# Kernel tuning notes

Measured on AMD Instinct MI355X. Metric: run time of the kernel, lower is better.

Reference implementation:

```python
import jax, jax.numpy as jnp
import numpy as np

BATCH = 64
FEAT = 2048          # backbone.out_features (ResNet-50)
C = 112              # bottleneck_dim = number of concepts
E = 512              # concept_emb_dim
NUM_CLASSES = 345


def setup_inputs() -> dict:
    key = jax.random.key(0)
    ks = jax.random.split(key, 7)
    s_emb = 1.0 / np.sqrt(FEAT)
    s_p = 1.0 / np.sqrt(2 * E)
    s_h = 1.0 / np.sqrt(C * E)
    return {
        "x": jax.random.normal(ks[0], (BATCH, FEAT), jnp.float32),
        "W_emb": jax.random.normal(ks[1], (C, FEAT, 2 * E), jnp.float32) * s_emb,
        "b_emb": jax.random.normal(ks[2], (C, 2 * E), jnp.float32) * s_emb,
        "W_pint": jax.random.normal(ks[3], (C, 2 * E), jnp.float32) * s_p,
        "b_pint": jax.random.normal(ks[4], (C,), jnp.float32) * s_p,
        "W_head": jax.random.normal(ks[5], (C * E, NUM_CLASSES), jnp.float32) * s_h,
        "b_head": jax.random.normal(ks[6], (NUM_CLASSES,), jnp.float32) * s_h,
    }


def reference(x, W_emb, b_emb, W_pint, b_pint, W_head, b_head):
    # Batched version of the per-concept Linear loop: [B,C,2E]
    embeddings = jnp.einsum("bf,cfe->bce", x, W_emb) + b_emb
    positive_embs = embeddings[..., :E]   # [B,C,E]
    negative_embs = embeddings[..., E:]   # [B,C,E]
    # Per-concept Linear(2E, 1) -> [B,C]
    p_int_logits = jnp.einsum("bce,ce->bc", embeddings, W_pint) + b_pint
    p_int_pos = jax.nn.sigmoid(p_int_logits)              # [B,C]
    p = p_int_pos[..., None]
    mixed_embs = p * positive_embs + (1.0 - p) * negative_embs  # [B,C,E]
    flattened = mixed_embs.reshape(mixed_embs.shape[0], -1)     # [B, C*E]
    final_preds = flattened @ W_head + b_head                   # [B, num_classes]
    return (final_preds, flattened, p_int_pos)
```

## Files before the change

### kernel.cpp

```cpp
#include <hip/hip_runtime.h>

typedef __attribute__((ext_vector_type(4))) float  f4;
typedef __attribute__((ext_vector_type(8))) short  bf16x8;
typedef __attribute__((ext_vector_type(4))) float  f32x4;
typedef __attribute__((ext_vector_type(4))) unsigned short us4;
typedef __attribute__((ext_vector_type(2))) unsigned int u32x2;

#define BATCH 64
#define FEAT 2048
#define NC_C 112
#define TE 1024
#define EE 512
#define NCLS 345
#define NCLSP 352
#define KHEAD 57344

__device__ __forceinline__ unsigned short f2bf(float f) {
    unsigned u = __float_as_uint(f);
    unsigned r = (u + 0x7FFFu + ((u >> 16) & 1u)) >> 16;
    return (unsigned short)r;
}
__device__ __forceinline__ float bf2f(unsigned short h) {
    return __uint_as_float(((unsigned)h) << 16);
}
__device__ __forceinline__ unsigned cvtpk(float a, float b) {
    unsigned r;
    asm("v_cvt_pk_bf16_f32 %0, %1, %2" : "=v"(r) : "v"(a), "v"(b));
    return r;
}

__global__ __launch_bounds__(256) void k_emb(
    const float* __restrict__ x, const float* __restrict__ W_emb,
    const float* __restrict__ b_emb, unsigned short* __restrict__ emb_bf)
{
    __shared__ __align__(16) unsigned short Alds[64 * 40];
    __shared__ __align__(16) unsigned short Blds[128 * 40];

    const int tid = threadIdx.x;
    const int c  = blockIdx.x >> 3;
    const int n0 = (blockIdx.x & 7) * 128;
    const float* __restrict__ Wc = W_emb + (size_t)c * (FEAT * TE);

    const int w = tid >> 6, l = tid & 63;
    const int mbase = (w & 1) * 32, nbase = (w >> 1) * 64;

    const int a_row = tid >> 3;
    const int a_k4  = (tid & 7) * 4;
    const int b_kp  = tid >> 4;
    const int b_n4  = (tid & 15) * 4;

    const float* __restrict__ axp = x + (size_t)a_row * FEAT + a_k4;
    const float* __restrict__ bpp = Wc + (size_t)(2 * b_kp) * TE + n0 + b_n4;

    unsigned short* __restrict__ aw0 = &Alds[a_row * 40 + a_k4];
    unsigned short* __restrict__ aw1 = &Alds[(a_row + 32) * 40 + a_k4];
    const int koct = b_kp >> 2, klo = (2 * b_kp) & 7;

    auto ke_load = [&](f4& A0, f4& A1, f4& B0, f4& B1, f4& B2, f4& B3, int kstep) {
        const float* ax_ = axp + kstep * 32;
        A0 = *(const f4*)ax_;
        A1 = *(const f4*)(ax_ + 32 * FEAT);
        const float* bp_ = bpp + (size_t)kstep * 32 * TE;
        B0 = *(const f4*)bp_;         B1 = *(const f4*)(bp_ + TE);
        B2 = *(const f4*)(bp_ + 64);  B3 = *(const f4*)(bp_ + TE + 64);
    };
    auto ke_write = [&](const f4& A0, const f4& A1, const f4& B0, const f4& B1,
                        const f4& B2, const f4& B3) {
        u32x2 v0, v1;
        v0[0] = cvtpk(A0[0], A0[1]); v0[1] = cvtpk(A0[2], A0[3]);
        v1[0] = cvtpk(A1[0], A1[1]); v1[1] = cvtpk(A1[2], A1[3]);
        *(u32x2*)aw0 = v0;
        *(u32x2*)aw1 = v1;
#pragma unroll
        for (int i = 0; i < 4; ++i) {
            int n = b_n4 + i;
            *(unsigned*)&Blds[n * 40 + (((koct ^ ((n >> 2) & 3)) << 3) | klo)] =
                cvtpk(B0[i], B1[i]);
            n += 64;
            *(unsigned*)&Blds[n * 40 + (((koct ^ ((n >> 2) & 3)) << 3) | klo)] =
                cvtpk(B2[i], B3[i]);
        }
    };

    f32x4 acc[2][4];
#pragma unroll
    for (int i = 0; i < 2; ++i)
#pragma unroll
        for (int j = 0; j < 4; ++j) acc[i][j] = (f32x4){0.f, 0.f, 0.f, 0.f};

    auto ke_mfma = [&]() {
        bf16x8 af[2], bfr[4];
#pragma unroll
        for (int si = 0; si < 2; ++si)
            af[si] = *(const bf16x8*)&Alds[(mbase + si * 16 + (l & 15)) * 40 + (l >> 4) * 8];
#pragma unroll
        for (int nf = 0; nf < 4; ++nf) {
            int n = nbase + nf * 16 + (l & 15);
            bfr[nf] = *(const bf16x8*)&Blds[n * 40 + (((l >> 4) ^ ((n >> 2) & 3)) << 3)];
        }
#pragma unroll
        for (int si = 0; si < 2; ++si)
#pragma unroll
            for (int nf = 0; nf < 4; ++nf)
                acc[si][nf] = __builtin_amdgcn_mfma_f32_16x16x32_bf16(
                    af[si], bfr[nf], acc[si][nf], 0, 0, 0);
    };

    f4 aA0, aA1, bA0, bA1, bA2, bA3;
    f4 aB0, aB1, bB0, bB1, bB2, bB3;
    ke_load(aA0, aA1, bA0, bA1, bA2, bA3, 0);
    ke_load(aB0, aB1, bB0, bB1, bB2, bB3, 1);

    for (int s = 0; s < 64; s += 2) {
        __syncthreads();
        ke_write(aA0, aA1, bA0, bA1, bA2, bA3);
        __syncthreads();
        if (s < 62) ke_load(aA0, aA1, bA0, bA1, bA2, bA3, s + 2);
        ke_mfma();

        __syncthreads();
        ke_write(aB0, aB1, bB0, bB1, bB2, bB3);
        __syncthreads();
        if (s < 61) ke_load(aB0, aB1, bB0, bB1, bB2, bB3, s + 3);
        ke_mfma();
    }

#pragma unroll
    for (int si = 0; si < 2; ++si)
#pragma unroll
        for (int nf = 0; nf < 4; ++nf) {
            const int nl = nbase + nf * 16 + (l & 15);
            const int ng = n0 + nl;
            const float bias = b_emb[c * TE + ng];
#pragma unroll
            for (int r = 0; r < 4; ++r) {
                const int bb = mbase + si * 16 + (l >> 4) * 4 + r;
                const float v = acc[si][nf][r] + bias;
                emb_bf[((size_t)bb * NC_C + c) * TE + ng] = f2bf(v);
            }
        }
}

__global__ __launch_bounds__(256) void k_mix(
    const unsigned short* __restrict__ emb_bf, const float* __restrict__ W_pint,
    const float* __restrict__ b_pint, float* __restrict__ flat_out,
    float* __restrict__ p_out)
{
    const int tid = threadIdx.x;
    const int l = tid & 63, w = tid >> 6;
    const int pidx = blockIdx.x * 4 + w;
    const int b = pidx / NC_C, c = pidx - b * NC_C;

    const unsigned short* __restrict__ row = emb_bf + ((size_t)b * NC_C + c) * TE;
    const float* __restrict__ wp = W_pint + c * TE;

    float vals[16];
    float dot = 0.f;
#pragma unroll
    for (int i = 0; i < 4; ++i) {
        const int e = 4 * l + 256 * i;
        us4 u = *(const us4*)&row[e];
        f4  wv = *(const f4*)&wp[e];
#pragma unroll
        for (int j = 0; j < 4; ++j) {
            float f = bf2f(u[j]);
            vals[i * 4 + j] = f;
            dot += f * wv[j];
        }
    }
#pragma unroll
    for (int m = 32; m >= 1; m >>= 1) dot += __shfl_xor(dot, m);
    const float logit = dot + b_pint[c];
    const float p = 1.f / (1.f + __expf(-logit));
    if (l == 0) p_out[b * NC_C + c] = p;

    float* __restrict__ fo = flat_out + (size_t)b * KHEAD + c * EE;
#pragma unroll
    for (int i = 0; i < 2; ++i) {
        const int e = 4 * l + 256 * i;
        f4 m;
#pragma unroll
        for (int j = 0; j < 4; ++j)
            m[j] = p * vals[i * 4 + j] + (1.f - p) * vals[(i + 2) * 4 + j];
        *(f4*)&fo[e] = m;
    }
}

__global__ __launch_bounds__(256) void k_head(
    const float* __restrict__ flat, const float* __restrict__ W_head,
    float* __restrict__ pbuf, int nsteps)
{
    __shared__ __align__(16) unsigned short Blds[NCLSP * 40];

    const int tid = threadIdx.x;
    const int w = tid >> 6, l = tid & 63;
    const int k0 = blockIdx.x * (nsteps * 32);

    f32x4 acc[22];
#pragma unroll
    for (int i = 0; i < 22; ++i) acc[i] = (f32x4){0.f, 0.f, 0.f, 0.f};

    for (int s = 0; s < nsteps; ++s) {
        const int kb = k0 + s * 32;
        __syncthreads();
        for (int idx = tid; idx < 32 * NCLSP; idx += 256) {
            const int k = idx / NCLSP;
            const int n = idx - k * NCLSP;
            const float v = (n < NCLS) ? W_head[(size_t)(kb + k) * NCLS + n] : 0.f;
            Blds[n * 40 + ((((k >> 3) ^ ((n >> 2) & 3)) << 3) | (k & 7))] = f2bf(v);
        }
        __syncthreads();

        const float* __restrict__ ap =
            flat + (size_t)(w * 16 + (l & 15)) * KHEAD + kb + (l >> 4) * 8;
        f4 af0 = *(const f4*)ap;
        f4 af1 = *(const f4*)(ap + 4);
        bf16x8 a;
        unsigned p0 = cvtpk(af0[0], af0[1]), p1 = cvtpk(af0[2], af0[3]);
        unsigned p2 = cvtpk(af1[0], af1[1]), p3 = cvtpk(af1[2], af1[3]);
        a[0] = (short)(p0 & 0xFFFF); a[1] = (short)(p0 >> 16);
        a[2] = (short)(p1 & 0xFFFF); a[3] = (short)(p1 >> 16);
        a[4] = (short)(p2 & 0xFFFF); a[5] = (short)(p2 >> 16);
        a[6] = (short)(p3 & 0xFFFF); a[7] = (short)(p3 >> 16);

#pragma unroll
        for (int nf = 0; nf < 22; ++nf) {
            const int n = nf * 16 + (l & 15);
            bf16x8 bfr = *(const bf16x8*)&Blds[n * 40 + (((l >> 4) ^ ((n >> 2) & 3)) << 3)];
            acc[nf] = __builtin_amdgcn_mfma_f32_16x16x32_bf16(a, bfr, acc[nf], 0, 0, 0);
        }
    }

    float* __restrict__ pb = pbuf + (size_t)blockIdx.x * (64 * NCLSP);
#pragma unroll
    for (int nf = 0; nf < 22; ++nf) {
        const int n = nf * 16 + (l & 15);
#pragma unroll
        for (int r = 0; r < 4; ++r) {
            const int row = w * 16 + (l >> 4) * 4 + r;
            pb[row * NCLSP + n] = acc[nf][r];
        }
    }
}

__global__ __launch_bounds__(256) void k_reduce(
    const float* __restrict__ pbuf, const float* __restrict__ b_head,
    float* __restrict__ final_out, int nb)
{
    const int i = blockIdx.x * 256 + threadIdx.x;
    if (i >= BATCH * NCLS) return;
    const int m = i / NCLS, n = i - m * NCLS;
    float s = b_head[n];
    for (int p = 0; p < nb; ++p)
        s += pbuf[((size_t)p * 64 + m) * NCLSP + n];
    final_out[i] = s;
}

extern "C" void kernel_launch(void* const* d_in, const int* in_sizes, int n_in,
                              void* d_out, int out_size, void* d_ws, size_t ws_size,
                              hipStream_t stream) {
    const float* x      = (const float*)d_in[0];
    const float* W_emb  = (const float*)d_in[1];
    const float* b_emb  = (const float*)d_in[2];
    const float* W_pint = (const float*)d_in[3];
    const float* b_pint = (const float*)d_in[4];
    const float* W_head = (const float*)d_in[5];
    const float* b_head = (const float*)d_in[6];

    float* out       = (float*)d_out;
    float* final_out = out;
    float* flat      = out + BATCH * NCLS;
    float* p_out     = out + BATCH * NCLS + BATCH * KHEAD;

    unsigned short* emb_bf = (unsigned short*)d_ws;
    float* pbuf = (float*)d_ws;

    int NB, nsteps;
    const size_t need224 = (size_t)224 * 64 * NCLSP * sizeof(float);
    if (ws_size >= need224) { NB = 224; nsteps = 8; }
    else                    { NB = 128; nsteps = 14; }

    k_emb<<<NC_C * 8, 256, 0, stream>>>(x, W_emb, b_emb, emb_bf);
    k_mix<<<(BATCH * NC_C) / 4, 256, 0, stream>>>(emb_bf, W_pint, b_pint, flat, p_out);
    k_head<<<NB, 256, 0, stream>>>(flat, W_head, pbuf, nsteps);
    k_reduce<<<(BATCH * NCLS + 255) / 256, 256, 0, stream>>>(pbuf, b_head, final_out, NB);
}
```

Baseline: 432.5 us.

## Pre-cast x to bf16 and stream W_emb directly into MFMA registers without LDS

Adds a small kernel that converts x to bf16 once, then rewrites the embedding GEMM so each wave loads its MFMA operand fragments straight from global memory into registers. LDS staging and all __syncthreads in the main loop go away, and a register double-buffered prefetch replaces them. The goal is to remove barrier and LDS round-trip overhead in this W_emb-bandwidth-bound kernel. The cost is scalar strided 4-byte loads of W_emb (eight rows per lane), which may coalesce worse than the earlier vectorized f4 loads, plus one extra kernel launch.

```diff
diff --git a/kernel.cpp b/kernel.cpp
--- a/kernel.cpp
+++ b/kernel.cpp
@@ -4,7 +4,7 @@
 typedef __attribute__((ext_vector_type(8))) short  bf16x8;
 typedef __attribute__((ext_vector_type(4))) float  f32x4;
 typedef __attribute__((ext_vector_type(4))) unsigned short us4;
-typedef __attribute__((ext_vector_type(2))) unsigned int u32x2;
+typedef __attribute__((ext_vector_type(4))) unsigned int u32x4;
 
 #define BATCH 64
 #define FEAT 2048
@@ -29,113 +29,102 @@
     return r;
 }
 
+__global__ __launch_bounds__(256) void k_xcast(
+    const float* __restrict__ x, unsigned short* __restrict__ xb)
+{
+    const int i = blockIdx.x * 256 + threadIdx.x;
+    const f4 v0 = *(const f4*)&x[i * 8];
+    const f4 v1 = *(const f4*)&x[i * 8 + 4];
+    u32x4 o;
+    o[0] = cvtpk(v0[0], v0[1]);
+    o[1] = cvtpk(v0[2], v0[3]);
+    o[2] = cvtpk(v1[0], v1[1]);
+    o[3] = cvtpk(v1[2], v1[3]);
+    *(u32x4*)&xb[i * 8] = o;
+}
+
 __global__ __launch_bounds__(256) void k_emb(
-    const float* __restrict__ x, const float* __restrict__ W_emb,
+    const unsigned short* __restrict__ xb, const float* __restrict__ W_emb,
     const float* __restrict__ b_emb, unsigned short* __restrict__ emb_bf)
 {
-    __shared__ __align__(16) unsigned short Alds[64 * 40];
-    __shared__ __align__(16) unsigned short Blds[128 * 40];
-
     const int tid = threadIdx.x;
     const int c  = blockIdx.x >> 3;
     const int n0 = (blockIdx.x & 7) * 128;
     const float* __restrict__ Wc = W_emb + (size_t)c * (FEAT * TE);
 
     const int w = tid >> 6, l = tid & 63;
-    const int mbase = (w & 1) * 32, nbase = (w >> 1) * 64;
-
-    const int a_row = tid >> 3;
-    const int a_k4  = (tid & 7) * 4;
-    const int b_kp  = tid >> 4;
-    const int b_n4  = (tid & 15) * 4;
-
-    const float* __restrict__ axp = x + (size_t)a_row * FEAT + a_k4;
-    const float* __restrict__ bpp = Wc + (size_t)(2 * b_kp) * TE + n0 + b_n4;
-
-    unsigned short* __restrict__ aw0 = &Alds[a_row * 40 + a_k4];
-    unsigned short* __restrict__ aw1 = &Alds[(a_row + 32) * 40 + a_k4];
-    const int koct = b_kp >> 2, klo = (2 * b_kp) & 7;
-
-    auto ke_load = [&](f4& A0, f4& A1, f4& B0, f4& B1, f4& B2, f4& B3, int kstep) {
-        const float* ax_ = axp + kstep * 32;
-        A0 = *(const f4*)ax_;
-        A1 = *(const f4*)(ax_ + 32 * FEAT);
-        const float* bp_ = bpp + (size_t)kstep * 32 * TE;
-        B0 = *(const f4*)bp_;         B1 = *(const f4*)(bp_ + TE);
-        B2 = *(const f4*)(bp_ + 64);  B3 = *(const f4*)(bp_ + TE + 64);
+    const int lm = l & 15, kg = l >> 4;
+    const int colbase = n0 + w * 32 + lm;
+
+    const float* __restrict__ bp = Wc + (size_t)(kg * 8) * TE + colbase;
+    const unsigned short* __restrict__ ap = xb + (size_t)lm * FEAT + kg * 8;
+
+    f32x4 acc[4][2];
+#pragma unroll
+    for (int mf = 0; mf < 4; ++mf)
+#pragma unroll
+        for (int nf = 0; nf < 2; ++nf) acc[mf][nf] = (f32x4){0.f, 0.f, 0.f, 0.f};
+
+    auto loadB = [&](float* B, int s) {
+        const float* p = bp + (size_t)s * 32 * TE;
+#pragma unroll
+        for (int nf = 0; nf < 2; ++nf)
+#pragma unroll
+            for (int r = 0; r < 8; ++r)
+                B[nf * 8 + r] = p[(size_t)r * TE + nf * 16];
     };
-    auto ke_write = [&](const f4& A0, const f4& A1, const f4& B0, const f4& B1,
-                        const f4& B2, const f4& B3) {
-        u32x2 v0, v1;
-        v0[0] = cvtpk(A0[0], A0[1]); v0[1] = cvtpk(A0[2], A0[3]);
-        v1[0] = cvtpk(A1[0], A1[1]); v1[1] = cvtpk(A1[2], A1[3]);
-        *(u32x2*)aw0 = v0;
-        *(u32x2*)aw1 = v1;
-#pragma unroll
-        for (int i = 0; i < 4; ++i) {
-            int n = b_n4 + i;
-            *(unsigned*)&Blds[n * 40 + (((koct ^ ((n >> 2) & 3)) << 3) | klo)] =
-                cvtpk(B0[i], B1[i]);
-            n += 64;
-            *(unsigned*)&Blds[n * 40 + (((koct ^ ((n >> 2) & 3)) << 3) | klo)] =
-                cvtpk(B2[i], B3[i]);
-        }
+    auto loadA = [&](bf16x8* A, int s) {
+        const unsigned short* p = ap + s * 32;
+#pragma unroll
+        for (int mf = 0; mf < 4; ++mf)
+            A[mf] = *(const bf16x8*)(p + mf * 16 * FEAT);
     };
-
-    f32x4 acc[2][4];
-#pragma unroll
-    for (int i = 0; i < 2; ++i)
-#pragma unroll
-        for (int j = 0; j < 4; ++j) acc[i][j] = (f32x4){0.f, 0.f, 0.f, 0.f};
-
-    auto ke_mfma = [&]() {
-        bf16x8 af[2], bfr[4];
-#pragma unroll
-        for (int si = 0; si < 2; ++si)
-            af[si] = *(const bf16x8*)&Alds[(mbase + si * 16 + (l & 15)) * 40 + (l >> 4) * 8];
-#pragma unroll
-        for (int nf = 0; nf < 4; ++nf) {
-            int n = nbase + nf * 16 + (l & 15);
-            bfr[nf] = *(const bf16x8*)&Blds[n * 40 + (((l >> 4) ^ ((n >> 2) & 3)) << 3)];
-        }
-#pragma unroll
-        for (int si = 0; si < 2; ++si)
-#pragma unroll
-            for (int nf = 0; nf < 4; ++nf)
-                acc[si][nf] = __builtin_amdgcn_mfma_f32_16x16x32_bf16(
-                    af[si], bfr[nf], acc[si][nf], 0, 0, 0);
+    auto compute = [&](const float* B, const bf16x8* A) {
+        bf16x8 bfr[2];
+#pragma unroll
+        for (int nf = 0; nf < 2; ++nf) {
+            u32x4 q;
+            q[0] = cvtpk(B[nf * 8 + 0], B[nf * 8 + 1]);
+            q[1] = cvtpk(B[nf * 8 + 2], B[nf * 8 + 3]);
+            q[2] = cvtpk(B[nf * 8 + 4], B[nf * 8 + 5]);
+            q[3] = cvtpk(B[nf * 8 + 6], B[nf * 8 + 7]);
+            bfr[nf] = __builtin_bit_cast(bf16x8, q);
+        }
+#pragma unroll
+        for (int mf = 0; mf < 4; ++mf)
+#pragma unroll
+            for (int nf = 0; nf < 2; ++nf)
+                acc[mf][nf] = __builtin_amdgcn_mfma_f32_16x16x32_bf16(
+                    A[mf], bfr[nf], acc[mf][nf], 0, 0, 0);
     };
 
-    f4 aA0, aA1, bA0, bA1, bA2, bA3;
-    f4 aB0, aB1, bB0, bB1, bB2, bB3;
-    ke_load(aA0, aA1, bA0, bA1, bA2, bA3, 0);
-    ke_load(aB0, aB1, bB0, bB1, bB2, bB3, 1);
-
+    float   Bc[16], Bn[16];
+    bf16x8  Ac[4],  An[4];
+    loadB(Bc, 0);
+    loadA(Ac, 0);
+
+#pragma unroll 1
     for (int s = 0; s < 64; s += 2) {
-        __syncthreads();
-        ke_write(aA0, aA1, bA0, bA1, bA2, bA3);
-        __syncthreads();
-        if (s < 62) ke_load(aA0, aA1, bA0, bA1, bA2, bA3, s + 2);
-        ke_mfma();
-
-        __syncthreads();
-        ke_write(aB0, aB1, bB0, bB1, bB2, bB3);
-        __syncthreads();
-        if (s < 61) ke_load(aB0, aB1, bB0, bB1, bB2, bB3, s + 3);
-        ke_mfma();
-    }
-
-#pragma unroll
-    for (int si = 0; si < 2; ++si)
-#pragma unroll
-        for (int nf = 0; nf < 4; ++nf) {
-            const int nl = nbase + nf * 16 + (l & 15);
-            const int ng = n0 + nl;
+        loadB(Bn, s + 1);
+        loadA(An, s + 1);
+        compute(Bc, Ac);
+        if (s + 2 < 64) {
+            loadB(Bc, s + 2);
+            loadA(Ac, s + 2);
+        }
+        compute(Bn, An);
+    }
+
+#pragma unroll
+    for (int mf = 0; mf < 4; ++mf)
+#pragma unroll
+        for (int nf = 0; nf < 2; ++nf) {
+            const int ng = n0 + w * 32 + nf * 16 + lm;
             const float bias = b_emb[c * TE + ng];
 #pragma unroll
             for (int r = 0; r < 4; ++r) {
-                const int bb = mbase + si * 16 + (l >> 4) * 4 + r;
-                const float v = acc[si][nf][r] + bias;
+                const int bb = mf * 16 + kg * 4 + r;
+                const float v = acc[mf][nf][r] + bias;
                 emb_bf[((size_t)bb * NC_C + c) * TE + ng] = f2bf(v);
             }
         }
@@ -215,13 +204,10 @@
             flat + (size_t)(w * 16 + (l & 15)) * KHEAD + kb + (l >> 4) * 8;
         f4 af0 = *(const f4*)ap;
         f4 af1 = *(const f4*)(ap + 4);
-        bf16x8 a;
-        unsigned p0 = cvtpk(af0[0], af0[1]), p1 = cvtpk(af0[2], af0[3]);
-        unsigned p2 = cvtpk(af1[0], af1[1]), p3 = cvtpk(af1[2], af1[3]);
-        a[0] = (short)(p0 & 0xFFFF); a[1] = (short)(p0 >> 16);
-        a[2] = (short)(p1 & 0xFFFF); a[3] = (short)(p1 >> 16);
-        a[4] = (short)(p2 & 0xFFFF); a[5] = (short)(p2 >> 16);
-        a[6] = (short)(p3 & 0xFFFF); a[7] = (short)(p3 >> 16);
+        u32x4 pq;
+        pq[0] = cvtpk(af0[0], af0[1]); pq[1] = cvtpk(af0[2], af0[3]);
+        pq[2] = cvtpk(af1[0], af1[1]); pq[3] = cvtpk(af1[2], af1[3]);
+        bf16x8 a = __builtin_bit_cast(bf16x8, pq);
 
 #pragma unroll
         for (int nf = 0; nf < 22; ++nf) {
@@ -274,13 +260,15 @@
 
     unsigned short* emb_bf = (unsigned short*)d_ws;
     float* pbuf = (float*)d_ws;
+    unsigned short* xb = (unsigned short*)((char*)d_ws + (32u << 20));
 
     int NB, nsteps;
-    const size_t need224 = (size_t)224 * 64 * NCLSP * sizeof(float);
+    const size_t need224 = (size_t)224 * 64 * NCLSP * sizeof(float) + (32u << 20);
     if (ws_size >= need224) { NB = 224; nsteps = 8; }
     else                    { NB = 128; nsteps = 14; }
 
-    k_emb<<<NC_C * 8, 256, 0, stream>>>(x, W_emb, b_emb, emb_bf);
+    k_xcast<<<64, 256, 0, stream>>>(x, xb);
+    k_emb<<<NC_C * 8, 256, 0, stream>>>(xb, W_emb, b_emb, emb_bf);
     k_mix<<<(BATCH * NC_C) / 4, 256, 0, stream>>>(emb_bf, W_pint, b_pint, flat, p_out);
     k_head<<<NB, 256, 0, stream>>>(flat, W_head, pbuf, nsteps);
     k_reduce<<<(BATCH * NCLS + 255) / 256, 256, 0, stream>>>(pbuf, b_head, final_out, NB);
```

Result: slower. 512.3 us (+18.5%).

## Split-K the concept embedding GEMM and reduce partials in the mix kernel

Applied to the files above, without the earlier changes.

The embedding GEMM is split along FEAT into 8 slices, so the grid grows from 896 to 7168 blocks and each block runs only 8 K-steps instead of 64. Each slice writes a bf16 partial tile to workspace. The mix kernel sums the 8 partials, adds b_emb, and then does the sigmoid/mix as before. This targets low occupancy and long per-block serial loops in k_emb. The cost is roughly 117 MB of extra partial-sum write and read traffic, extra rounding from storing partials in bf16, and a hard-coded workspace layout with the ws_size check removed. A small cleanup also replaces the head kernel's A-fragment packing with a bitcast.

```diff
diff --git a/kernel.cpp b/kernel.cpp
--- a/kernel.cpp
+++ b/kernel.cpp
@@ -5,6 +5,7 @@
 typedef __attribute__((ext_vector_type(4))) float  f32x4;
 typedef __attribute__((ext_vector_type(4))) unsigned short us4;
 typedef __attribute__((ext_vector_type(2))) unsigned int u32x2;
+typedef __attribute__((ext_vector_type(4))) unsigned int u32x4;
 
 #define BATCH 64
 #define FEAT 2048
@@ -31,14 +32,18 @@
 
 __global__ __launch_bounds__(256) void k_emb(
     const float* __restrict__ x, const float* __restrict__ W_emb,
-    const float* __restrict__ b_emb, unsigned short* __restrict__ emb_bf)
+    unsigned short* __restrict__ pbe)
 {
     __shared__ __align__(16) unsigned short Alds[64 * 40];
     __shared__ __align__(16) unsigned short Blds[128 * 40];
 
     const int tid = threadIdx.x;
-    const int c  = blockIdx.x >> 3;
-    const int n0 = (blockIdx.x & 7) * 128;
+    const int bid = blockIdx.x;
+    const int c  = bid >> 6;
+    const int nt = (bid >> 3) & 7;
+    const int ks = bid & 7;
+    const int n0 = nt * 128;
+    const int kofs = ks * 256;
     const float* __restrict__ Wc = W_emb + (size_t)c * (FEAT * TE);
 
     const int w = tid >> 6, l = tid & 63;
@@ -49,8 +54,8 @@
     const int b_kp  = tid >> 4;
     const int b_n4  = (tid & 15) * 4;
 
-    const float* __restrict__ axp = x + (size_t)a_row * FEAT + a_k4;
-    const float* __restrict__ bpp = Wc + (size_t)(2 * b_kp) * TE + n0 + b_n4;
+    const float* __restrict__ axp = x + (size_t)a_row * FEAT + kofs + a_k4;
+    const float* __restrict__ bpp = Wc + (size_t)(kofs + 2 * b_kp) * TE + n0 + b_n4;
 
     unsigned short* __restrict__ aw0 = &Alds[a_row * 40 + a_k4];
     unsigned short* __restrict__ aw1 = &Alds[(a_row + 32) * 40 + a_k4];
@@ -106,22 +111,14 @@
                     af[si], bfr[nf], acc[si][nf], 0, 0, 0);
     };
 
-    f4 aA0, aA1, bA0, bA1, bA2, bA3;
-    f4 aB0, aB1, bB0, bB1, bB2, bB3;
-    ke_load(aA0, aA1, bA0, bA1, bA2, bA3, 0);
-    ke_load(aB0, aB1, bB0, bB1, bB2, bB3, 1);
-
-    for (int s = 0; s < 64; s += 2) {
-        __syncthreads();
-        ke_write(aA0, aA1, bA0, bA1, bA2, bA3);
-        __syncthreads();
-        if (s < 62) ke_load(aA0, aA1, bA0, bA1, bA2, bA3, s + 2);
-        ke_mfma();
-
-        __syncthreads();
-        ke_write(aB0, aB1, bB0, bB1, bB2, bB3);
-        __syncthreads();
-        if (s < 61) ke_load(aB0, aB1, bB0, bB1, bB2, bB3, s + 3);
+    f4 a0, a1, p0, p1, p2, p3;
+    ke_load(a0, a1, p0, p1, p2, p3, 0);
+
+    for (int s = 0; s < 8; ++s) {
+        __syncthreads();
+        ke_write(a0, a1, p0, p1, p2, p3);
+        __syncthreads();
+        if (s < 7) ke_load(a0, a1, p0, p1, p2, p3, s + 1);
         ke_mfma();
     }
 
@@ -131,42 +128,50 @@
         for (int nf = 0; nf < 4; ++nf) {
             const int nl = nbase + nf * 16 + (l & 15);
             const int ng = n0 + nl;
-            const float bias = b_emb[c * TE + ng];
 #pragma unroll
             for (int r = 0; r < 4; ++r) {
-                const int bb = mbase + si * 16 + (l >> 4) * 4 + r;
-                const float v = acc[si][nf][r] + bias;
-                emb_bf[((size_t)bb * NC_C + c) * TE + ng] = f2bf(v);
+                const int m = mbase + si * 16 + (l >> 4) * 4 + r;
+                pbe[((size_t)(ks * 64 + m) * NC_C + c) * TE + ng] = f2bf(acc[si][nf][r]);
             }
         }
 }
 
 __global__ __launch_bounds__(256) void k_mix(
-    const unsigned short* __restrict__ emb_bf, const float* __restrict__ W_pint,
-    const float* __restrict__ b_pint, float* __restrict__ flat_out,
-    float* __restrict__ p_out)
+    const unsigned short* __restrict__ pbe, const float* __restrict__ b_emb,
+    const float* __restrict__ W_pint, const float* __restrict__ b_pint,
+    float* __restrict__ flat_out, float* __restrict__ p_out)
 {
     const int tid = threadIdx.x;
     const int l = tid & 63, w = tid >> 6;
     const int pidx = blockIdx.x * 4 + w;
     const int b = pidx / NC_C, c = pidx - b * NC_C;
 
-    const unsigned short* __restrict__ row = emb_bf + ((size_t)b * NC_C + c) * TE;
+    float vals[16];
+#pragma unroll
+    for (int i = 0; i < 4; ++i) {
+        const f4 bi = *(const f4*)&b_emb[c * TE + 4 * l + 256 * i];
+#pragma unroll
+        for (int j = 0; j < 4; ++j) vals[4 * i + j] = bi[j];
+    }
+#pragma unroll
+    for (int ksl = 0; ksl < 8; ++ksl) {
+        const unsigned short* __restrict__ rp =
+            pbe + ((size_t)(ksl * 64 + b) * NC_C + c) * TE;
+#pragma unroll
+        for (int i = 0; i < 4; ++i) {
+            us4 u = *(const us4*)&rp[4 * l + 256 * i];
+#pragma unroll
+            for (int j = 0; j < 4; ++j) vals[4 * i + j] += bf2f(u[j]);
+        }
+    }
+
     const float* __restrict__ wp = W_pint + c * TE;
-
-    float vals[16];
     float dot = 0.f;
 #pragma unroll
     for (int i = 0; i < 4; ++i) {
-        const int e = 4 * l + 256 * i;
-        us4 u = *(const us4*)&row[e];
-        f4  wv = *(const f4*)&wp[e];
-#pragma unroll
-        for (int j = 0; j < 4; ++j) {
-            float f = bf2f(u[j]);
-            vals[i * 4 + j] = f;
-            dot += f * wv[j];
-        }
+        const f4 wv = *(const f4*)&wp[4 * l + 256 * i];
+#pragma unroll
+        for (int j = 0; j < 4; ++j) dot += vals[4 * i + j] * wv[j];
     }
 #pragma unroll
     for (int m = 32; m >= 1; m >>= 1) dot += __shfl_xor(dot, m);
@@ -177,12 +182,11 @@
     float* __restrict__ fo = flat_out + (size_t)b * KHEAD + c * EE;
 #pragma unroll
     for (int i = 0; i < 2; ++i) {
-        const int e = 4 * l + 256 * i;
         f4 m;
 #pragma unroll
         for (int j = 0; j < 4; ++j)
             m[j] = p * vals[i * 4 + j] + (1.f - p) * vals[(i + 2) * 4 + j];
-        *(f4*)&fo[e] = m;
+        *(f4*)&fo[4 * l + 256 * i] = m;
     }
 }
 
@@ -215,13 +219,10 @@
             flat + (size_t)(w * 16 + (l & 15)) * KHEAD + kb + (l >> 4) * 8;
         f4 af0 = *(const f4*)ap;
         f4 af1 = *(const f4*)(ap + 4);
-        bf16x8 a;
-        unsigned p0 = cvtpk(af0[0], af0[1]), p1 = cvtpk(af0[2], af0[3]);
-        unsigned p2 = cvtpk(af1[0], af1[1]), p3 = cvtpk(af1[2], af1[3]);
-        a[0] = (short)(p0 & 0xFFFF); a[1] = (short)(p0 >> 16);
-        a[2] = (short)(p1 & 0xFFFF); a[3] = (short)(p1 >> 16);
-        a[4] = (short)(p2 & 0xFFFF); a[5] = (short)(p2 >> 16);
-        a[6] = (short)(p3 & 0xFFFF); a[7] = (short)(p3 >> 16);
+        u32x4 pq;
+        pq[0] = cvtpk(af0[0], af0[1]); pq[1] = cvtpk(af0[2], af0[3]);
+        pq[2] = cvtpk(af1[0], af1[1]); pq[3] = cvtpk(af1[2], af1[3]);
+        bf16x8 a = __builtin_bit_cast(bf16x8, pq);
 
 #pragma unroll
         for (int nf = 0; nf < 22; ++nf) {
@@ -272,16 +273,13 @@
     float* flat      = out + BATCH * NCLS;
     float* p_out     = out + BATCH * NCLS + BATCH * KHEAD;
 
-    unsigned short* emb_bf = (unsigned short*)d_ws;
-    float* pbuf = (float*)d_ws;
-
-    int NB, nsteps;
-    const size_t need224 = (size_t)224 * 64 * NCLSP * sizeof(float);
-    if (ws_size >= need224) { NB = 224; nsteps = 8; }
-    else                    { NB = 128; nsteps = 14; }
-
-    k_emb<<<NC_C * 8, 256, 0, stream>>>(x, W_emb, b_emb, emb_bf);
-    k_mix<<<(BATCH * NC_C) / 4, 256, 0, stream>>>(emb_bf, W_pint, b_pint, flat, p_out);
-    k_head<<<NB, 256, 0, stream>>>(flat, W_head, pbuf, nsteps);
-    k_reduce<<<(BATCH * NCLS + 255) / 256, 256, 0, stream>>>(pbuf, b_head, final_out, NB);
-}
+    unsigned short* pbe = (unsigned short*)d_ws;
+    float* pbuf_h = (float*)((char*)d_ws + (size_t)120 * 1024 * 1024);
+
+    const int NB = 224, nsteps = 8;
+
+    k_emb<<<NC_C * 8 * 8, 256, 0, stream>>>(x, W_emb, pbe);
+    k_mix<<<(BATCH * NC_C) / 4, 256, 0, stream>>>(pbe, b_emb, W_pint, b_pint, flat, p_out);
+    k_head<<<NB, 256, 0, stream>>>(flat, W_head, pbuf_h, nsteps);
+    k_reduce<<<(BATCH * NCLS + 255) / 256, 256, 0, stream>>>(pbuf_h, b_head, final_out, NB);
+}
```

Result: slower. 478.7 us (+10.7%).
